# Kernel tuning notes

Measured on AMD Instinct MI355X. Metric: run time of the kernel, lower is better.

The kernel has to match this reference:

```python
import jax, jax.numpy as jnp
import numpy as np

B, L, D, H, NL = 4, 2048, 128, 4, 2
DH = D // H
FF = 2 * D
EPS_LN = 1e-5


def _p(key, shape, scale=0.05):
    return (jax.random.normal(key, shape, dtype=jnp.float32) * scale)


def setup_inputs() -> dict:
    key = jax.random.key(0)
    ks = jax.random.split(key, 40)
    inp = {
        "local_global": jax.random.normal(ks[0], (B, D), dtype=jnp.float32),
        "task_features": jax.random.normal(ks[1], (B, L, 15), dtype=jnp.float32),
        "privacy_features": jax.random.normal(ks[2], (B, L, 6), dtype=jnp.float32),
        "dag_features": jax.random.normal(ks[3], (B, L, 4), dtype=jnp.float32),
        # float mask in [0,1); values > 0.5 are MASKED (set to -inf) per torch code
        "attn_mask": jax.random.uniform(ks[4], (B, L, L), dtype=jnp.float32),
        # input projections (stored [in, out]; torch Linear does x @ W.T + b)
        "task_W": _p(ks[5], (15, D)), "task_b": jnp.zeros((D,), jnp.float32),
        "priv_W": _p(ks[6], (6, D)), "priv_b": jnp.zeros((D,), jnp.float32),
        "dag_W": _p(ks[7], (4, D)), "dag_b": jnp.zeros((D,), jnp.float32),
        "pre_g": jnp.ones((D,), jnp.float32), "pre_b": jnp.zeros((D,), jnp.float32),
        "post_g": jnp.ones((D,), jnp.float32), "post_b": jnp.zeros((D,), jnp.float32),
        "out_W": _p(ks[8], (D, D)), "out_b": jnp.zeros((D,), jnp.float32),
        # per-layer params stacked on leading NL axis
        "qW": _p(ks[9], (NL, D, D)), "qb": jnp.zeros((NL, D), jnp.float32),
        "kW": _p(ks[10], (NL, D, D)), "kb": jnp.zeros((NL, D), jnp.float32),
        "vW": _p(ks[11], (NL, D, D)), "vb": jnp.zeros((NL, D), jnp.float32),
        "oW": _p(ks[12], (NL, D, D)), "ob": jnp.zeros((NL, D), jnp.float32),
        "n1g": jnp.ones((NL, D), jnp.float32), "n1b": jnp.zeros((NL, D), jnp.float32),
        "n2g": jnp.ones((NL, D), jnp.float32), "n2b": jnp.zeros((NL, D), jnp.float32),
        "f1W": _p(ks[13], (NL, D, FF)), "f1b": jnp.zeros((NL, FF), jnp.float32),
        "f2W": _p(ks[14], (NL, FF, D)), "f2b": jnp.zeros((NL, D), jnp.float32),
    }
    return inp


def _layernorm(x, g, b):
    mu = x.mean(-1, keepdims=True)
    var = ((x - mu) ** 2).mean(-1, keepdims=True)
    return (x - mu) * jax.lax.rsqrt(var + EPS_LN) * g + b


def _attention(x, add_mask, Wq, bq, Wk, bk, Wv, bv, Wo, bo):
    # x: [B,L,D]; add_mask: [B,L,L] additive (0 or -inf)
    def heads(y):
        return y.reshape(B, L, H, DH).transpose(0, 2, 1, 3)  # [B,H,L,DH]
    q = heads(x @ Wq + bq)
    k = heads(x @ Wk + bk)
    v = heads(x @ Wv + bv)
    scale = 1.0 / np.sqrt(DH).astype(np.float32)
    scores = jnp.einsum('bhqd,bhkd->bhqk', q, k) * scale + add_mask[:, None]
    # fully-masked-row diagonal fixup (torch: set diag score to 0 where row max is -inf)
    row_max = scores.max(-1)                       # [B,H,L]
    fully_masked = jnp.isinf(row_max) & (row_max < 0)
    eye = jnp.eye(L, dtype=bool)
    scores = jnp.where(fully_masked[..., None] & eye, 0.0, scores)
    w = jax.nn.softmax(scores, axis=-1)
    # NaN fallback: if any NaN, replace with 1/L and renormalize (applied globally, as torch does)
    has_nan = jnp.isnan(w).any()
    fixed = jnp.nan_to_num(w, nan=1.0 / L)
    fixed = fixed / (fixed.sum(-1, keepdims=True) + 1e-8)
    w = jnp.where(has_nan, fixed, w)
    out = jnp.einsum('bhqk,bhkd->bhqd', w, v)      # [B,H,L,DH]
    out = out.transpose(0, 2, 1, 3).reshape(B, L, D)
    return out @ Wo + bo


def reference(local_global, task_features, privacy_features, dag_features, attn_mask,
              task_W, task_b, priv_W, priv_b, dag_W, dag_b,
              pre_g, pre_b, post_g, post_b, out_W, out_b,
              qW, qb, kW, kb, vW, vb, oW, ob,
              n1g, n1b, n2g, n2b, f1W, f1b, f2W, f2b):
    # normalize mask: >0.5 means masked; fix all-False rows by masking their diagonal (torch quirk)
    mb = attn_mask > 0.5                            # [B,L,L] bool, True = mask out
    need_fix = ~mb.any(-1)                          # [B,L]
    eye = jnp.eye(L, dtype=bool)
    mb = mb | (need_fix[..., None] & eye)
    add_mask = jnp.where(mb, -jnp.inf, 0.0).astype(jnp.float32)

    ctx = (task_features @ task_W + task_b) + (privacy_features @ priv_W + priv_b) \
          + (dag_features @ dag_W + dag_b)
    x = _layernorm(ctx, pre_g, pre_b)
    for i in range(NL):  # eval mode: dropout = identity
        sa = _attention(_layernorm(x, n1g[i], n1b[i]), add_mask,
                        qW[i], qb[i], kW[i], kb[i], vW[i], vb[i], oW[i], ob[i])
        x = x + sa
        h = _layernorm(x, n2g[i], n2b[i])
        ff = jax.nn.gelu(h @ f1W[i] + f1b[i], approximate=False) @ f2W[i] + f2b[i]
        x = x + ff
    enc = _layernorm(x, post_g, post_b)
    global_ctx = enc.mean(axis=1)                   # [B,D]
    fused = global_ctx + 0.1 * local_global
    aligned = fused @ out_W + out_b
    return aligned
```

## Files before the change

kernel.cpp:

```cpp
#include <hip/hip_runtime.h>
#include <hip/hip_bf16.h>

#define DEV __device__ __forceinline__

typedef float f32x4 __attribute__((ext_vector_type(4)));
typedef float f32x16 __attribute__((ext_vector_type(16)));
typedef short s16x8 __attribute__((ext_vector_type(8)));
typedef unsigned short u16x4 __attribute__((ext_vector_type(4)));
typedef __bf16 bf16x8 __attribute__((ext_vector_type(8)));

DEV bf16x8 as_bf16(s16x8 v) { return __builtin_bit_cast(bf16x8, v); }

DEV unsigned short f2bf(float f) {
    union { __hip_bfloat16 h; unsigned short u; } c;
    c.h = __float2bfloat16(f);
    return c.u;
}

DEV unsigned f2bf2(float lo, float hi) {
    unsigned ulo = __builtin_bit_cast(unsigned, lo);
    unsigned uhi = __builtin_bit_cast(unsigned, hi);
    ulo = (ulo + 0x7fffu + ((ulo >> 16) & 1u)) >> 16;
    uhi = (uhi + 0x7fffu + ((uhi >> 16) & 1u)) & 0xffff0000u;
    return ulo | uhi;
// ... 167 lines not shown
        for (int ns = 0; ns < 4; ++ns) {
            const int n = n0 + ns * 16 + c16;
            const float bv = bias[n];
            u16x4 pk;
#pragma unroll
            for (int r = 0; r < 4; ++r) pk[r] = f2bf(acc[ns][r] + bv);
            *(u16x4*)&vtbuf[(size_t)(n - 256) * 8192 + row0] = pk;
        }
        return;
    }
#pragma unroll
    for (int ns = 0; ns < 4; ++ns) {
        const int n = n0 + ns * 16 + c16;
        const float bv = bias[n];
#pragma unroll
        for (int r = 0; r < 4; ++r)
            qk[(size_t)(m0 + 4 * g + r) * 256 + n] = f2bf(acc[ns][r] + bv);
    }
}

__global__ __launch_bounds__(512) void gace_flash7_k(
    const unsigned short* __restrict__ QK,
    const unsigned short* __restrict__ Vt,
    const unsigned long long* __restrict__ bits,
    float* __restrict__ Op, float* __restrict__ ml)
{
    __shared__ __align__(16) unsigned short Ks[2 * 2 * 2560];
    __shared__ __align__(16) char VtB[2 * 2 * 4096];

    const int tid = threadIdx.x;
    const int wid = tid >> 6, l = tid & 63;
    const int c32 = l & 31, hi = l >> 5;
    const int bid = (blockIdx.x & 7) * 64 + (blockIdx.x >> 3);
    const int split = bid & 3, qc = (bid >> 2) & 7, h = (bid >> 5) & 3, b = bid >> 7;
    const size_t base = (size_t)b * 2048;
    const int qb0 = qc * 256 + wid * 32;
    const int q = qb0 + c32;

    const unsigned short* qrow = &QK[(base + q) * 256 + h * 32];
    const s16x8 qf0 = *(const s16x8*)&qrow[8 * hi];
    const s16x8 qf1 = *(const s16x8*)&qrow[16 + 8 * hi];
    const int rot3c = rot3(c32 & 7);

    f32x16 oacc;
#pragma unroll
    for (int i = 0; i < 16; ++i) oacc[i] = 0.f;
    float l_ = 0.f;

    const int st = tid & 255;
    const int sr = st >> 2;
    const int se = (tid & 3) << 3;
    const int lowr = sr & 31, t12 = lowr & 12;
    const int prow = (sr & 32) | (((t12 == 4) | (t12 == 8)) ? (lowr ^ 12) : lowr);
    const int rv = st >> 3;
    const int sv = tid & 7;
    const int vds = rv * 128 + 16 * (sv ^ rot3(rv & 7));

    const int kv0 = split * 512;
    const unsigned long long* bq = &bits[(base + q) * 32 + split * 8];
    const unsigned short* kgb = &QK[base * 256 + 128 + h * 32 + se];
    const unsigned short* vgb = &Vt[(size_t)(h * 32 + rv) * 8192 + base + kv0 + sv * 8];

    s16x8 kregA, kregB, vregA, vregB;
    auto LOAD = [&](int it2) {
        if (tid < 256) {
            const int kv = kv0 + it2 * 128;
            kregA = *(const s16x8*)&kgb[(size_t)(kv + sr) * 256];
            kregB = *(const s16x8*)&kgb[(size_t)(kv + 64 + sr) * 256];
        } else {
            vregA = *(const s16x8*)&vgb[it2 * 128];
            vregB = *(const s16x8*)&vgb[it2 * 128 + 64];
        }
    };
    auto STAGE = [&](int pb) {
        if (tid < 256) {
            *(s16x8*)&Ks[(pb * 2 + 0) * 2560 + prow * 40 + se] = kregA;
            *(s16x8*)&Ks[(pb * 2 + 1) * 2560 + prow * 40 + se] = kregB;
        } else {
            *(s16x8*)&VtB[(pb * 2 + 0) * 4096 + vds] = vregA;
            *(s16x8*)&VtB[(pb * 2 + 1) * 4096 + vds] = vregB;
        }
    };
    auto COMPUTE = [&](int pb, int sub, unsigned long long wb) {
        const unsigned short* KsS = &Ks[(pb * 2 + sub) * 2560];
        const char* VtS = &VtB[(pb * 2 + sub) * 4096];
        const unsigned long long wbs = wb >> (8 * hi);
        const unsigned wlo = (unsigned)wbs, whiw = (unsigned)(wbs >> 32);
        __builtin_amdgcn_s_setprio(1);
#pragma unroll
        for (int H = 0; H < 2; ++H) {
            const unsigned short* kr = &KsS[(32 * H + c32) * 40 + 8 * hi];
            f32x16 zv;
#pragma unroll
            for (int i = 0; i < 16; ++i) zv[i] = 0.f;
            f32x16 sac = __builtin_amdgcn_mfma_f32_32x32x16_bf16(
                as_bf16(*(const s16x8*)&kr[0]), as_bf16(qf0), zv, 0, 0, 0);
            sac = __builtin_amdgcn_mfma_f32_32x32x16_bf16(
                as_bf16(*(const s16x8*)&kr[16]), as_bf16(qf1), sac, 0, 0, 0);
            const unsigned word = (H == 0) ? wlo : whiw;
#pragma unroll
            for (int ch = 0; ch < 2; ++ch) {
                const int c = 2 * H + ch;
                const int bb = ch * 16;
                float p[8];
#pragma unroll
                for (int e = 0; e < 8; ++e) {
                    const float pe = exp2f(sac[ch * 8 + e]);
                    p[e] = ((word >> (bb + e)) & 1u) ? 0.f : pe;
                }
                l_ += ((p[0] + p[1]) + (p[2] + p[3])) + ((p[4] + p[5]) + (p[6] + p[7]));
                union { s16x8 v; unsigned d[4]; } pa;
#pragma unroll
                for (int j = 0; j < 4; ++j)
                    asm("v_cvt_pk_bf16_f32 %0, %1, %2"
                        : "=v"(pa.d[j]) : "v"(p[2 * j]), "v"(p[2 * j + 1]));
                const s16x8 vf = *(const s16x8*)&VtS[c32 * 128 + 16 * ((2 * c + hi) ^ rot3c)];
                oacc = __builtin_amdgcn_mfma_f32_32x32x16_bf16(
                    as_bf16(pa.v), as_bf16(vf), oacc, 0, 0, 0);
            }
        }
        __builtin_amdgcn_s_setprio(0);
    };

    unsigned long long wbv[8];
#pragma unroll
    for (int w = 0; w < 8; ++w) wbv[w] = bq[w];
    LOAD(0);
    STAGE(0);
    LOAD(1);
    __syncthreads();

#pragma unroll
    for (int it = 0; it < 4; ++it) {
        const int p = it & 1;
        COMPUTE(p, 0, wbv[2 * it]);
        if (it < 3) {
            STAGE(p ^ 1);
            if (it < 2) LOAD(it + 2);
        }
        COMPUTE(p, 1, wbv[2 * it + 1]);
        if (it < 3) __syncthreads();
    }

    l_ += __shfl_xor(l_, 32, 64);
    float* orow = &Op[((size_t)split * 8192 + base + qb0) * 128 + h * 32 + c32];
#pragma unroll
    for (int r = 0; r < 16; ++r) {
        const int qoff = (r & 3) + 8 * (r >> 2) + 4 * hi;
        orow[(size_t)qoff * 128] = oacc[r];
    }
    if (l < 32) ml[((size_t)split * 8192 + base + q) * 4 + h] = l_;
}

template<int LAST>
__global__ __launch_bounds__(128) void gace_post_k(
    const float* __restrict__ Op, const float* __restrict__ ml,
    const unsigned short* __restrict__ oWt, const float* __restrict__ obv,
    float* __restrict__ x,
    const float* __restrict__ n2g, const float* __restrict__ n2b,
    const unsigned short* __restrict__ f1Wt, const float* __restrict__ f1b,
    const unsigned short* __restrict__ f2Wt, const float* __restrict__ f2b,
    const float* __restrict__ post_g, const float* __restrict__ post_b,
    float* __restrict__ partial)
{
    __shared__ __align__(16) float xbuf[2][16][132];
    __shared__ __align__(16) unsigned short g1buf[2][16][264];
    __shared__ float red[2][128];
    const int tid = threadIdx.x, wid = tid >> 6, l = tid & 63;
    const int g = (l >> 4) & 3, c16 = l & 15;
    const int m0 = blockIdx.x * 32 + wid * 16;
    const int arow = m0 + c16;

    s16x8 af[4];
#pragma unroll
    for (int kc = 0; kc < 4; ++kc) {
        float o[8];
#pragma unroll
        for (int e = 0; e < 8; ++e) o[e] = 0.f;
        float Ls = 0.f;
#pragma unroll
        for (int sp = 0; sp < 4; ++sp) {
            const size_t ro = (size_t)sp * 8192 + arow;
            const f32x4 a0 = *(const f32x4*)&Op[ro * 128 + kc * 32 + 8 * g];
            const f32x4 a1 = *(const f32x4*)&Op[ro * 128 + kc * 32 + 8 * g + 4];
#pragma unroll
            for (int e = 0; e < 4; ++e) { o[e] += a0[e]; o[4 + e] += a1[e]; }
            Ls += ml[ro * 4 + kc];
        }
        const float inv = 1.f / Ls;
        union { s16x8 v8; unsigned d[4]; } pk;
#pragma unroll
        for (int j = 0; j < 4; ++j) pk.d[j] = f2bf2(o[2 * j] * inv, o[2 * j + 1] * inv);
        af[kc] = pk.v8;
    }
    f32x4 acc8[8];
#pragma unroll
    for (int i = 0; i < 8; ++i) acc8[i] = f32x4{0.f, 0.f, 0.f, 0.f};
#pragma unroll
    for (int ns = 0; ns < 8; ++ns) {
        const unsigned short* wrow = oWt + (size_t)(16 * ns + c16) * 128;
#pragma unroll
        for (int kc = 0; kc < 4; ++kc)
            acc8[ns] = __builtin_amdgcn_mfma_f32_16x16x32_bf16(
                as_bf16(af[kc]), as_bf16(*(const s16x8*)&wrow[kc * 32 + 8 * g]),
                acc8[ns], 0, 0, 0);
    }
#pragma unroll
    for (int ns = 0; ns < 8; ++ns) {
        const int n = 16 * ns + c16;
        const float bv = obv[n];
#pragma unroll
        for (int r = 0; r < 4; ++r) {
            const int lr = 4 * g + r;
            xbuf[wid][lr][n] = acc8[ns][r] + bv + x[(size_t)(m0 + lr) * 128 + n];
        }
    }
    float v2[4][8];
#pragma unroll
    for (int kc = 0; kc < 4; ++kc) {
        const f32x4 a0 = *(const f32x4*)&xbuf[wid][c16][kc * 32 + 8 * g];
        const f32x4 a1 = *(const f32x4*)&xbuf[wid][c16][kc * 32 + 8 * g + 4];
#pragma unroll
        for (int e = 0; e < 4; ++e) { v2[kc][e] = a0[e]; v2[kc][4 + e] = a1[e]; }
    }
    float s = 0.f;
#pragma unroll
    for (int kc = 0; kc < 4; ++kc)
#pragma unroll
        for (int e = 0; e < 8; ++e) s += v2[kc][e];
    s += __shfl_xor(s, 16, 64); s += __shfl_xor(s, 32, 64);
    const float mean = s * (1.f / 128.f);
    float s2 = 0.f;
#pragma unroll
    for (int kc = 0; kc < 4; ++kc)
#pragma unroll
        for (int e = 0; e < 8; ++e) { const float d = v2[kc][e] - mean; s2 += d * d; }
    s2 += __shfl_xor(s2, 16, 64); s2 += __shfl_xor(s2, 32, 64);
    const float rs = rsqrtf(s2 * (1.f / 128.f) + 1e-5f);
    s16x8 af1[4];
#pragma unroll
    for (int kc = 0; kc < 4; ++kc) {
        union { s16x8 v8; unsigned d[4]; } pk;
#pragma unroll
        for (int j = 0; j < 4; ++j) {
            const int col = kc * 32 + 8 * g + 2 * j;
            const float x0 = (v2[kc][2 * j] - mean) * rs * n2g[col] + n2b[col];
            const float x1 = (v2[kc][2 * j + 1] - mean) * rs * n2g[col + 1] + n2b[col + 1];
            pk.d[j] = f2bf2(x0, x1);
        }
        af1[kc] = pk.v8;
    }
    f32x4 acc16[16];
#pragma unroll
    for (int i = 0; i < 16; ++i) acc16[i] = f32x4{0.f, 0.f, 0.f, 0.f};
#pragma unroll
    for (int ns = 0; ns < 16; ++ns) {
        const unsigned short* wrow = f1Wt + (size_t)(16 * ns + c16) * 128;
#pragma unroll
        for (int kc = 0; kc < 4; ++kc)
            acc16[ns] = __builtin_amdgcn_mfma_f32_16x16x32_bf16(
                as_bf16(af1[kc]), as_bf16(*(const s16x8*)&wrow[kc * 32 + 8 * g]),
                acc16[ns], 0, 0, 0);
    }
#pragma unroll
    for (int ns = 0; ns < 16; ++ns) {
        const int n = 16 * ns + c16;
        const float bv = f1b[n];
#pragma unroll
        for (int r = 0; r < 4; ++r) {
            float vv = acc16[ns][r] + bv;
            vv = vv * 0.5f * (1.0f + erff(vv * 0.70710678118654752f));
            g1buf[wid][4 * g + r][n] = f2bf(vv);
        }
    }
    s16x8 af2[8];
#pragma unroll
    for (int kc = 0; kc < 8; ++kc)
        af2[kc] = *(const s16x8*)&g1buf[wid][c16][kc * 32 + 8 * g];
    f32x4 acc8b[8];
#pragma unroll
    for (int i = 0; i < 8; ++i) acc8b[i] = f32x4{0.f, 0.f, 0.f, 0.f};
#pragma unroll
    for (int ns = 0; ns < 8; ++ns) {
        const unsigned short* wrow = f2Wt + (size_t)(16 * ns + c16) * 256;
#pragma unroll
        for (int kc = 0; kc < 8; ++kc)
            acc8b[ns] = __builtin_amdgcn_mfma_f32_16x16x32_bf16(
                as_bf16(af2[kc]), as_bf16(*(const s16x8*)&wrow[kc * 32 + 8 * g]),
                acc8b[ns], 0, 0, 0);
    }
    float fx[8][4];
#pragma unroll
    for (int ns = 0; ns < 8; ++ns) {
        const int n = 16 * ns + c16;
        const float bv = f2b[n];
#pragma unroll
        for (int r = 0; r < 4; ++r)
            fx[ns][r] = acc8b[ns][r] + bv + xbuf[wid][4 * g + r][n];
    }
    if (!LAST) {
#pragma unroll
        for (int ns = 0; ns < 8; ++ns) {
            const int n = 16 * ns + c16;
#pragma unroll
            for (int r = 0; r < 4; ++r)
                x[(size_t)(m0 + 4 * g + r) * 128 + n] = fx[ns][r];
        }
        return;
    }
    float colsum[8];
#pragma unroll
    for (int ns = 0; ns < 8; ++ns) colsum[ns] = 0.f;
#pragma unroll
    for (int r = 0; r < 4; ++r) {
        float sr_ = 0.f;
#pragma unroll
        for (int ns = 0; ns < 8; ++ns) sr_ += fx[ns][r];
        sr_ += __shfl_xor(sr_, 1, 64); sr_ += __shfl_xor(sr_, 2, 64);
        sr_ += __shfl_xor(sr_, 4, 64); sr_ += __shfl_xor(sr_, 8, 64);
        const float mr = sr_ * (1.f / 128.f);
        float vr = 0.f;
#pragma unroll
        for (int ns = 0; ns < 8; ++ns) { const float d = fx[ns][r] - mr; vr += d * d; }
        vr += __shfl_xor(vr, 1, 64); vr += __shfl_xor(vr, 2, 64);
        vr += __shfl_xor(vr, 4, 64); vr += __shfl_xor(vr, 8, 64);
        const float rsr = rsqrtf(vr * (1.f / 128.f) + 1e-5f);
#pragma unroll
        for (int ns = 0; ns < 8; ++ns) {
            const int n = 16 * ns + c16;
            colsum[ns] += (fx[ns][r] - mr) * rsr * post_g[n] + post_b[n];
        }
    }
#pragma unroll
    for (int ns = 0; ns < 8; ++ns) {
        colsum[ns] += __shfl_xor(colsum[ns], 16, 64);
        colsum[ns] += __shfl_xor(colsum[ns], 32, 64);
    }
    if (l < 16) {
#pragma unroll
        for (int ns = 0; ns < 8; ++ns) red[wid][16 * ns + c16] = colsum[ns];
    }
    __syncthreads();
    if (tid < 128)
        partial[(size_t)blockIdx.x * 128 + tid] = red[0][tid] + red[1][tid];
}

__global__ __launch_bounds__(128) void gace_tailB_k(
    const float* __restrict__ partial, const float* __restrict__ lg,
    const float* __restrict__ oW, const float* __restrict__ obv,
    float* __restrict__ out)
{
    const int tid = threadIdx.x, b2 = blockIdx.x;
    __shared__ float fused[128];
    float s = 0.f;
#pragma unroll 8
    for (int c = 0; c < 64; ++c) s += partial[(size_t)(b2 * 64 + c) * 128 + tid];
    fused[tid] = s * (1.f / 2048.f) + 0.1f * lg[b2 * 128 + tid];
    __syncthreads();
    float r = obv[tid];
#pragma unroll 8
    for (int d2 = 0; d2 < 128; ++d2) r += fused[d2] * oW[d2 * 128 + tid];
    out[b2 * 128 + tid] = r;
}

extern "C" void kernel_launch(void* const* d_in, const int* in_sizes, int n_in,
                              void* d_out, int out_size, void* d_ws, size_t ws_size,
                              hipStream_t stream)
{
    (void)in_sizes; (void)n_in; (void)out_size; (void)ws_size;
    const float* local_global = (const float*)d_in[0];
    const float* task   = (const float*)d_in[1];
    const float* priv   = (const float*)d_in[2];
    const float* dag    = (const float*)d_in[3];
    const float* amask  = (const float*)d_in[4];
    const float* task_W = (const float*)d_in[5];
    const float* task_b = (const float*)d_in[6];
    const float* priv_W = (const float*)d_in[7];
    const float* priv_b = (const float*)d_in[8];
    const float* dag_W  = (const float*)d_in[9];
    const float* dag_b  = (const float*)d_in[10];
    const float* pre_g  = (const float*)d_in[11];
    const float* pre_b  = (const float*)d_in[12];
    const float* post_g = (const float*)d_in[13];
    const float* post_b = (const float*)d_in[14];
    const float* out_W  = (const float*)d_in[15];
    const float* out_b  = (const float*)d_in[16];
    const float* qW = (const float*)d_in[17];
    const float* qb = (const float*)d_in[18];
    const float* kW = (const float*)d_in[19];
    const float* kb = (const float*)d_in[20];
    const float* vW = (const float*)d_in[21];
    const float* vb = (const float*)d_in[22];
    const float* oW = (const float*)d_in[23];
    const float* ob = (const float*)d_in[24];
    const float* n1g = (const float*)d_in[25];
    const float* n1b = (const float*)d_in[26];
    const float* n2g = (const float*)d_in[27];
    const float* n2b = (const float*)d_in[28];
    const float* f1W = (const float*)d_in[29];
    const float* f1b = (const float*)d_in[30];
    const float* f2W = (const float*)d_in[31];
    const float* f2b = (const float*)d_in[32];

    char* ws = (char*)d_ws;
    size_t off = 0;
    auto carve = [&](size_t sz) {
        void* p = ws + off;
        off += (sz + 255) & ~(size_t)255;
        return p;
    };
    unsigned long long* bits = (unsigned long long*)carve(8192ull * 32 * 8);
    float*          x    = (float*)carve(8192ull * 128 * 4);
    unsigned short* qk   = (unsigned short*)carve(8192ull * 256 * 2);
    unsigned short* vt   = (unsigned short*)carve(128ull * 8192 * 2);
    float*          part = (float*)carve(256ull * 128 * 4);
    float*          Op   = (float*)carve(4ull * 8192 * 128 * 4);
    float*          mlb  = (float*)carve(4ull * 8192 * 4 * 4);
    unsigned short* wbf  = (unsigned short*)carve(2ull * 131072 * 2);
    float*          bcat = (float*)carve(2ull * 384 * 4);

    gace_setup_k<<<5888, 256, 0, stream>>>(
        amask, bits,
        task, priv, dag, task_W, task_b, priv_W, priv_b, dag_W, dag_b,
        pre_g, pre_b, x,
        qW, kW, vW, oW, f1W, f2W, qb, kb, vb, wbf, bcat);
    for (int i = 0; i < 2; ++i) {
        const unsigned short* wl = wbf + (size_t)i * 131072;
        gace_qkv_k<<<dim3(128, 6), 256, 0, stream>>>(
            x, n1g + i * 128, n1b + i * 128, wl, bcat + i * 384, qk, vt);
        gace_flash7_k<<<512, 512, 0, stream>>>(qk, vt, bits, Op, mlb);
        if (i == 0)
            gace_post_k<0><<<256, 128, 0, stream>>>(
                Op, mlb, wl + 49152, ob, x, n2g, n2b,
                wl + 65536, f1b, wl + 98304, f2b, post_g, post_b, part);
        else
            gace_post_k<1><<<256, 128, 0, stream>>>(
                Op, mlb, wl + 49152, ob + 128, x, n2g + 128, n2b + 128,
                wl + 65536, f1b + 256, wl + 98304, f2b + 128, post_g, post_b, part);
    }
    gace_tailB_k<<<4, 128, 0, stream>>>(part, local_global, out_W, out_b, (float*)d_out);
}
```

Measured before the change: 175.5 us.

## Fuse layer-0 post-attention MLP with layer-1 LayerNorm and QKV projection

Adds a kernel that, after the layer-0 attention merge, out-projection and FFN, also computes the layer-1 LayerNorm and QKV projection for its rows and writes q/k and transposed v directly. This removes one kernel launch and the re-read of x by a separate QKV kernel between layers. The fused kernel runs on only 256 blocks of 128 threads, so the QKV work gets less parallelism than the dedicated 128x6 grid had. Register pressure also rises in the longer kernel.

New measurement: 169.7 us. 3.3% less time.

```diff
diff --git a/kernel.cpp b/kernel.cpp
--- a/kernel.cpp
+++ b/kernel.cpp
@@ -343,7 +343,229 @@
     if (l < 32) ml[((size_t)split * 8192 + base + q) * 4 + h] = l_;
 }
 
-template<int LAST>
+__global__ __launch_bounds__(128) void gace_postqkv_k(
+    const float* __restrict__ Op, const float* __restrict__ ml,
+    const unsigned short* __restrict__ oWt, const float* __restrict__ obv,
+    float* __restrict__ x,
+    const float* __restrict__ n2g, const float* __restrict__ n2b,
+    const unsigned short* __restrict__ f1Wt, const float* __restrict__ f1b,
+    const unsigned short* __restrict__ f2Wt, const float* __restrict__ f2b,
+    const float* __restrict__ n1g2, const float* __restrict__ n1b2,
+    const unsigned short* __restrict__ w2,
+    const float* __restrict__ bcat2,
+    unsigned short* __restrict__ qk, unsigned short* __restrict__ vtbuf)
+{
+    __shared__ __align__(16) float xbuf[2][16][132];
+    __shared__ __align__(16) unsigned short g1buf[2][16][264];
+    const int tid = threadIdx.x, wid = tid >> 6, l = tid & 63;
+    const int g = (l >> 4) & 3, c16 = l & 15;
+    const int m0 = blockIdx.x * 32 + wid * 16;
+    const int arow = m0 + c16;
+
+    s16x8 af[4];
+#pragma unroll
+    for (int kc = 0; kc < 4; ++kc) {
+        float o[8];
+#pragma unroll
+        for (int e = 0; e < 8; ++e) o[e] = 0.f;
+        float Ls = 0.f;
+#pragma unroll
+        for (int sp = 0; sp < 4; ++sp) {
+            const size_t ro = (size_t)sp * 8192 + arow;
+            const f32x4 a0 = *(const f32x4*)&Op[ro * 128 + kc * 32 + 8 * g];
+            const f32x4 a1 = *(const f32x4*)&Op[ro * 128 + kc * 32 + 8 * g + 4];
+#pragma unroll
+            for (int e = 0; e < 4; ++e) { o[e] += a0[e]; o[4 + e] += a1[e]; }
+            Ls += ml[ro * 4 + kc];
+        }
+        const float inv = 1.f / Ls;
+        union { s16x8 v8; unsigned d[4]; } pk;
+#pragma unroll
+        for (int j = 0; j < 4; ++j) pk.d[j] = f2bf2(o[2 * j] * inv, o[2 * j + 1] * inv);
+        af[kc] = pk.v8;
+    }
+    f32x4 acc8[8];
+#pragma unroll
+    for (int i = 0; i < 8; ++i) acc8[i] = f32x4{0.f, 0.f, 0.f, 0.f};
+#pragma unroll
+    for (int ns = 0; ns < 8; ++ns) {
+        const unsigned short* wrow = oWt + (size_t)(16 * ns + c16) * 128;
+#pragma unroll
+        for (int kc = 0; kc < 4; ++kc)
+            acc8[ns] = __builtin_amdgcn_mfma_f32_16x16x32_bf16(
+                as_bf16(af[kc]), as_bf16(*(const s16x8*)&wrow[kc * 32 + 8 * g]),
+                acc8[ns], 0, 0, 0);
+    }
+#pragma unroll
+    for (int ns = 0; ns < 8; ++ns) {
+        const int n = 16 * ns + c16;
+        const float bv = obv[n];
+#pragma unroll
+        for (int r = 0; r < 4; ++r) {
+            const int lr = 4 * g + r;
+            xbuf[wid][lr][n] = acc8[ns][r] + bv + x[(size_t)(m0 + lr) * 128 + n];
+        }
+    }
+    float v2[4][8];
+#pragma unroll
+    for (int kc = 0; kc < 4; ++kc) {
+        const f32x4 a0 = *(const f32x4*)&xbuf[wid][c16][kc * 32 + 8 * g];
+        const f32x4 a1 = *(const f32x4*)&xbuf[wid][c16][kc * 32 + 8 * g + 4];
+#pragma unroll
+        for (int e = 0; e < 4; ++e) { v2[kc][e] = a0[e]; v2[kc][4 + e] = a1[e]; }
+    }
+    float s = 0.f;
+#pragma unroll
+    for (int kc = 0; kc < 4; ++kc)
+#pragma unroll
+        for (int e = 0; e < 8; ++e) s += v2[kc][e];
+    s += __shfl_xor(s, 16, 64); s += __shfl_xor(s, 32, 64);
+    const float mean = s * (1.f / 128.f);
+    float s2 = 0.f;
+#pragma unroll
+    for (int kc = 0; kc < 4; ++kc)
+#pragma unroll
+        for (int e = 0; e < 8; ++e) { const float d = v2[kc][e] - mean; s2 += d * d; }
+    s2 += __shfl_xor(s2, 16, 64); s2 += __shfl_xor(s2, 32, 64);
+    const float rs = rsqrtf(s2 * (1.f / 128.f) + 1e-5f);
+    s16x8 af1[4];
+#pragma unroll
+    for (int kc = 0; kc < 4; ++kc) {
+        union { s16x8 v8; unsigned d[4]; } pk;
+#pragma unroll
+        for (int j = 0; j < 4; ++j) {
+            const int col = kc * 32 + 8 * g + 2 * j;
+            const float x0 = (v2[kc][2 * j] - mean) * rs * n2g[col] + n2b[col];
+            const float x1 = (v2[kc][2 * j + 1] - mean) * rs * n2g[col + 1] + n2b[col + 1];
+            pk.d[j] = f2bf2(x0, x1);
+        }
+        af1[kc] = pk.v8;
+    }
+    f32x4 acc16[16];
+#pragma unroll
+    for (int i = 0; i < 16; ++i) acc16[i] = f32x4{0.f, 0.f, 0.f, 0.f};
+#pragma unroll
+    for (int ns = 0; ns < 16; ++ns) {
+        const unsigned short* wrow = f1Wt + (size_t)(16 * ns + c16) * 128;
+#pragma unroll
+        for (int kc = 0; kc < 4; ++kc)
+            acc16[ns] = __builtin_amdgcn_mfma_f32_16x16x32_bf16(
+                as_bf16(af1[kc]), as_bf16(*(const s16x8*)&wrow[kc * 32 + 8 * g]),
+                acc16[ns], 0, 0, 0);
+    }
+#pragma unroll
+    for (int ns = 0; ns < 16; ++ns) {
+        const int n = 16 * ns + c16;
+        const float bv = f1b[n];
+#pragma unroll
+        for (int r = 0; r < 4; ++r) {
+            float vv = acc16[ns][r] + bv;
+            vv = vv * 0.5f * (1.0f + erff(vv * 0.70710678118654752f));
+            g1buf[wid][4 * g + r][n] = f2bf(vv);
+        }
+    }
+    s16x8 af2[8];
+#pragma unroll
+    for (int kc = 0; kc < 8; ++kc)
+        af2[kc] = *(const s16x8*)&g1buf[wid][c16][kc * 32 + 8 * g];
+    f32x4 acc8b[8];
+#pragma unroll
+    for (int i = 0; i < 8; ++i) acc8b[i] = f32x4{0.f, 0.f, 0.f, 0.f};
+#pragma unroll
+    for (int ns = 0; ns < 8; ++ns) {
+        const unsigned short* wrow = f2Wt + (size_t)(16 * ns + c16) * 256;
+#pragma unroll
+        for (int kc = 0; kc < 8; ++kc)
+            acc8b[ns] = __builtin_amdgcn_mfma_f32_16x16x32_bf16(
+                as_bf16(af2[kc]), as_bf16(*(const s16x8*)&wrow[kc * 32 + 8 * g]),
+                acc8b[ns], 0, 0, 0);
+    }
+#pragma unroll
+    for (int ns = 0; ns < 8; ++ns) {
+        const int n = 16 * ns + c16;
+        const float bv = f2b[n];
+#pragma unroll
+        for (int r = 0; r < 4; ++r) {
+            const int lr = 4 * g + r;
+            const float fxv = acc8b[ns][r] + bv + xbuf[wid][lr][n];
+            x[(size_t)(m0 + lr) * 128 + n] = fxv;
+            xbuf[wid][lr][n] = fxv;
+        }
+    }
+    float v1[4][8];
+#pragma unroll
+    for (int kc = 0; kc < 4; ++kc) {
+        const f32x4 a0 = *(const f32x4*)&xbuf[wid][c16][kc * 32 + 8 * g];
+        const f32x4 a1 = *(const f32x4*)&xbuf[wid][c16][kc * 32 + 8 * g + 4];
+#pragma unroll
+        for (int e = 0; e < 4; ++e) { v1[kc][e] = a0[e]; v1[kc][4 + e] = a1[e]; }
+    }
+    float s1 = 0.f;
+#pragma unroll
+    for (int kc = 0; kc < 4; ++kc)
+#pragma unroll
+        for (int e = 0; e < 8; ++e) s1 += v1[kc][e];
+    s1 += __shfl_xor(s1, 16, 64); s1 += __shfl_xor(s1, 32, 64);
+    const float mean1 = s1 * (1.f / 128.f);
+    float sq1 = 0.f;
+#pragma unroll
+    for (int kc = 0; kc < 4; ++kc)
+#pragma unroll
+        for (int e = 0; e < 8; ++e) { const float d = v1[kc][e] - mean1; sq1 += d * d; }
+    sq1 += __shfl_xor(sq1, 16, 64); sq1 += __shfl_xor(sq1, 32, 64);
+    const float rs1 = rsqrtf(sq1 * (1.f / 128.f) + 1e-5f);
+    s16x8 afq[4];
+#pragma unroll
+    for (int kc = 0; kc < 4; ++kc) {
+        union { s16x8 v8; unsigned d[4]; } pk;
+#pragma unroll
+        for (int j = 0; j < 4; ++j) {
+            const int col = kc * 32 + 8 * g + 2 * j;
+            const float x0 = (v1[kc][2 * j] - mean1) * rs1 * n1g2[col] + n1b2[col];
+            const float x1 = (v1[kc][2 * j + 1] - mean1) * rs1 * n1g2[col + 1] + n1b2[col + 1];
+            pk.d[j] = f2bf2(x0, x1);
+        }
+        afq[kc] = pk.v8;
+    }
+#pragma unroll
+    for (int nt = 0; nt < 6; ++nt) {
+        const int n0 = nt * 64;
+        f32x4 acc[4];
+#pragma unroll
+        for (int z = 0; z < 4; ++z) acc[z] = f32x4{0.f, 0.f, 0.f, 0.f};
+#pragma unroll
+        for (int ns = 0; ns < 4; ++ns) {
+            const unsigned short* wrow = w2 + (size_t)(n0 + 16 * ns + c16) * 128;
+#pragma unroll
+            for (int kc = 0; kc < 4; ++kc)
+                acc[ns] = __builtin_amdgcn_mfma_f32_16x16x32_bf16(
+                    as_bf16(afq[kc]), as_bf16(*(const s16x8*)&wrow[kc * 32 + 8 * g]),
+                    acc[ns], 0, 0, 0);
+        }
+        if (n0 >= 256) {
+            const int row0 = m0 + 4 * g;
+#pragma unroll
+            for (int ns = 0; ns < 4; ++ns) {
+                const int n = n0 + ns * 16 + c16;
+                const float bv = bcat2[n];
+                u16x4 pk;
+#pragma unroll
+                for (int r = 0; r < 4; ++r) pk[r] = f2bf(acc[ns][r] + bv);
+                *(u16x4*)&vtbuf[(size_t)(n - 256) * 8192 + row0] = pk;
+            }
+        } else {
+#pragma unroll
+            for (int ns = 0; ns < 4; ++ns) {
+                const int n = n0 + ns * 16 + c16;
+                const float bv = bcat2[n];
+#pragma unroll
+                for (int r = 0; r < 4; ++r)
+                    qk[(size_t)(m0 + 4 * g + r) * 256 + n] = f2bf(acc[ns][r] + bv);
+            }
+        }
+    }
+}
+
 __global__ __launch_bounds__(128) void gace_post_k(
     const float* __restrict__ Op, const float* __restrict__ ml,
     const unsigned short* __restrict__ oWt, const float* __restrict__ obv,
@@ -488,16 +710,6 @@
 #pragma unroll
         for (int r = 0; r < 4; ++r)
             fx[ns][r] = acc8b[ns][r] + bv + xbuf[wid][4 * g + r][n];
-    }
-    if (!LAST) {
-#pragma unroll
-        for (int ns = 0; ns < 8; ++ns) {
-            const int n = 16 * ns + c16;
-#pragma unroll
-            for (int r = 0; r < 4; ++r)
-                x[(size_t)(m0 + 4 * g + r) * 128 + n] = fx[ns][r];
-        }
-        return;
     }
     float colsum[8];
 #pragma unroll
@@ -615,19 +827,17 @@
         task, priv, dag, task_W, task_b, priv_W, priv_b, dag_W, dag_b,
         pre_g, pre_b, x,
         qW, kW, vW, oW, f1W, f2W, qb, kb, vb, wbf, bcat);
-    for (int i = 0; i < 2; ++i) {
-        const unsigned short* wl = wbf + (size_t)i * 131072;
-        gace_qkv_k<<<dim3(128, 6), 256, 0, stream>>>(
-            x, n1g + i * 128, n1b + i * 128, wl, bcat + i * 384, qk, vt);
-        gace_flash7_k<<<512, 512, 0, stream>>>(qk, vt, bits, Op, mlb);
-        if (i == 0)
-            gace_post_k<0><<<256, 128, 0, stream>>>(
-                Op, mlb, wl + 49152, ob, x, n2g, n2b,
-                wl + 65536, f1b, wl + 98304, f2b, post_g, post_b, part);
-        else
-            gace_post_k<1><<<256, 128, 0, stream>>>(
-                Op, mlb, wl + 49152, ob + 128, x, n2g + 128, n2b + 128,
-                wl + 65536, f1b + 256, wl + 98304, f2b + 128, post_g, post_b, part);
-    }
+    gace_qkv_k<<<dim3(128, 6), 256, 0, stream>>>(
+        x, n1g, n1b, wbf, bcat, qk, vt);
+    gace_flash7_k<<<512, 512, 0, stream>>>(qk, vt, bits, Op, mlb);
+    gace_postqkv_k<<<256, 128, 0, stream>>>(
+        Op, mlb, wbf + 49152, ob, x, n2g, n2b,
+        wbf + 65536, f1b, wbf + 98304, f2b,
+        n1g + 128, n1b + 128, wbf + 131072, bcat + 384, qk, vt);
+    gace_flash7_k<<<512, 512, 0, stream>>>(qk, vt, bits, Op, mlb);
+    gace_post_k<<<256, 128, 0, stream>>>(
+        Op, mlb, wbf + 131072 + 49152, ob + 128, x, n2g + 128, n2b + 128,
+        wbf + 131072 + 65536, f1b + 256, wbf + 131072 + 98304, f2b + 128,
+        post_g, post_b, part);
     gace_tailB_k<<<4, 128, 0, stream>>>(part, local_global, out_W, out_b, (float*)d_out);
 }
```

## Fuse layer-2 QKV projection into layer-1 post kernel and split N across waves

Applied to the files above, without the earlier changes.

The post-attention kernel now processes 16 rows per block with 4 waves that split the output columns, instead of each wave owning 16 rows with all columns. For layer 1 it also applies the next layer's LayerNorm and QKV projection, writing qk/vt directly and removing one separate QKV launch. The final LN and column-sum path is rewritten for the new layout, and the tail reduction now reads 128 partials per batch. This doubles the grid and adds block-level syncs in exchange for more parallelism and one fewer launch and x re-read.

Result: faster. 160.7 us (-8.5%).

```diff
diff --git a/kernel.cpp b/kernel.cpp
--- a/kernel.cpp
+++ b/kernel.cpp
@@ -343,23 +343,26 @@
     if (l < 32) ml[((size_t)split * 8192 + base + q) * 4 + h] = l_;
 }
 
-template<int LAST>
-__global__ __launch_bounds__(128) void gace_post_k(
+template<int QKV, int LAST>
+__global__ __launch_bounds__(256) void gace_post2_k(
     const float* __restrict__ Op, const float* __restrict__ ml,
     const unsigned short* __restrict__ oWt, const float* __restrict__ obv,
     float* __restrict__ x,
     const float* __restrict__ n2g, const float* __restrict__ n2b,
     const unsigned short* __restrict__ f1Wt, const float* __restrict__ f1b,
     const unsigned short* __restrict__ f2Wt, const float* __restrict__ f2b,
+    const float* __restrict__ n1g2, const float* __restrict__ n1b2,
+    const unsigned short* __restrict__ w2, const float* __restrict__ bcat2,
+    unsigned short* __restrict__ qk, unsigned short* __restrict__ vtbuf,
     const float* __restrict__ post_g, const float* __restrict__ post_b,
     float* __restrict__ partial)
 {
-    __shared__ __align__(16) float xbuf[2][16][132];
-    __shared__ __align__(16) unsigned short g1buf[2][16][264];
-    __shared__ float red[2][128];
+    __shared__ __align__(16) float xbuf[16][132];
+    __shared__ __align__(16) unsigned short g1buf[16][264];
+    __shared__ float stats[16][2];
     const int tid = threadIdx.x, wid = tid >> 6, l = tid & 63;
     const int g = (l >> 4) & 3, c16 = l & 15;
-    const int m0 = blockIdx.x * 32 + wid * 16;
+    const int m0 = blockIdx.x * 16;
     const int arow = m0 + c16;
 
     s16x8 af[4];
@@ -384,156 +387,238 @@
         for (int j = 0; j < 4; ++j) pk.d[j] = f2bf2(o[2 * j] * inv, o[2 * j + 1] * inv);
         af[kc] = pk.v8;
     }
-    f32x4 acc8[8];
-#pragma unroll
-    for (int i = 0; i < 8; ++i) acc8[i] = f32x4{0.f, 0.f, 0.f, 0.f};
-#pragma unroll
-    for (int ns = 0; ns < 8; ++ns) {
-        const unsigned short* wrow = oWt + (size_t)(16 * ns + c16) * 128;
+    {
+        f32x4 acc2[2];
+#pragma unroll
+        for (int z = 0; z < 2; ++z) acc2[z] = f32x4{0.f, 0.f, 0.f, 0.f};
+#pragma unroll
+        for (int nsl = 0; nsl < 2; ++nsl) {
+            const int ns = wid * 2 + nsl;
+            const unsigned short* wrow = oWt + (size_t)(16 * ns + c16) * 128;
+#pragma unroll
+            for (int kc = 0; kc < 4; ++kc)
+                acc2[nsl] = __builtin_amdgcn_mfma_f32_16x16x32_bf16(
+                    as_bf16(af[kc]), as_bf16(*(const s16x8*)&wrow[kc * 32 + 8 * g]),
+                    acc2[nsl], 0, 0, 0);
+        }
+#pragma unroll
+        for (int nsl = 0; nsl < 2; ++nsl) {
+            const int n = 16 * (wid * 2 + nsl) + c16;
+            const float bv = obv[n];
+#pragma unroll
+            for (int r = 0; r < 4; ++r) {
+                const int lr = 4 * g + r;
+                xbuf[lr][n] = acc2[nsl][r] + bv + x[(size_t)(m0 + lr) * 128 + n];
+            }
+        }
+    }
+    __syncthreads();
+    s16x8 af1[4];
+    {
+        float v2[4][8];
+#pragma unroll
+        for (int kc = 0; kc < 4; ++kc) {
+            const f32x4 a0 = *(const f32x4*)&xbuf[c16][kc * 32 + 8 * g];
+            const f32x4 a1 = *(const f32x4*)&xbuf[c16][kc * 32 + 8 * g + 4];
+#pragma unroll
+            for (int e = 0; e < 4; ++e) { v2[kc][e] = a0[e]; v2[kc][4 + e] = a1[e]; }
+        }
+        float s = 0.f;
 #pragma unroll
         for (int kc = 0; kc < 4; ++kc)
-            acc8[ns] = __builtin_amdgcn_mfma_f32_16x16x32_bf16(
-                as_bf16(af[kc]), as_bf16(*(const s16x8*)&wrow[kc * 32 + 8 * g]),
-                acc8[ns], 0, 0, 0);
-    }
-#pragma unroll
-    for (int ns = 0; ns < 8; ++ns) {
-        const int n = 16 * ns + c16;
-        const float bv = obv[n];
+#pragma unroll
+            for (int e = 0; e < 8; ++e) s += v2[kc][e];
+        s += __shfl_xor(s, 16, 64); s += __shfl_xor(s, 32, 64);
+        const float mean = s * (1.f / 128.f);
+        float s2 = 0.f;
+#pragma unroll
+        for (int kc = 0; kc < 4; ++kc)
+#pragma unroll
+            for (int e = 0; e < 8; ++e) { const float d = v2[kc][e] - mean; s2 += d * d; }
+        s2 += __shfl_xor(s2, 16, 64); s2 += __shfl_xor(s2, 32, 64);
+        const float rs = rsqrtf(s2 * (1.f / 128.f) + 1e-5f);
+#pragma unroll
+        for (int kc = 0; kc < 4; ++kc) {
+            union { s16x8 v8; unsigned d[4]; } pk;
+#pragma unroll
+            for (int j = 0; j < 4; ++j) {
+                const int col = kc * 32 + 8 * g + 2 * j;
+                const float x0 = (v2[kc][2 * j] - mean) * rs * n2g[col] + n2b[col];
+                const float x1 = (v2[kc][2 * j + 1] - mean) * rs * n2g[col + 1] + n2b[col + 1];
+                pk.d[j] = f2bf2(x0, x1);
+            }
+            af1[kc] = pk.v8;
+        }
+    }
+    {
+        f32x4 accf[4];
+#pragma unroll
+        for (int z = 0; z < 4; ++z) accf[z] = f32x4{0.f, 0.f, 0.f, 0.f};
+#pragma unroll
+        for (int nsl = 0; nsl < 4; ++nsl) {
+            const int ns = wid * 4 + nsl;
+            const unsigned short* wrow = f1Wt + (size_t)(16 * ns + c16) * 128;
+#pragma unroll
+            for (int kc = 0; kc < 4; ++kc)
+                accf[nsl] = __builtin_amdgcn_mfma_f32_16x16x32_bf16(
+                    as_bf16(af1[kc]), as_bf16(*(const s16x8*)&wrow[kc * 32 + 8 * g]),
+                    accf[nsl], 0, 0, 0);
+        }
+#pragma unroll
+        for (int nsl = 0; nsl < 4; ++nsl) {
+            const int n = 16 * (wid * 4 + nsl) + c16;
+            const float bv = f1b[n];
+#pragma unroll
+            for (int r = 0; r < 4; ++r) {
+                float vv = accf[nsl][r] + bv;
+                vv = vv * 0.5f * (1.0f + erff(vv * 0.70710678118654752f));
+                g1buf[4 * g + r][n] = f2bf(vv);
+            }
+        }
+    }
+    __syncthreads();
+    float fx[2][4];
+    {
+        s16x8 af2[8];
+#pragma unroll
+        for (int kc = 0; kc < 8; ++kc)
+            af2[kc] = *(const s16x8*)&g1buf[c16][kc * 32 + 8 * g];
+        f32x4 acc2[2];
+#pragma unroll
+        for (int z = 0; z < 2; ++z) acc2[z] = f32x4{0.f, 0.f, 0.f, 0.f};
+#pragma unroll
+        for (int nsl = 0; nsl < 2; ++nsl) {
+            const int ns = wid * 2 + nsl;
+            const unsigned short* wrow = f2Wt + (size_t)(16 * ns + c16) * 256;
+#pragma unroll
+            for (int kc = 0; kc < 8; ++kc)
+                acc2[nsl] = __builtin_amdgcn_mfma_f32_16x16x32_bf16(
+                    as_bf16(af2[kc]), as_bf16(*(const s16x8*)&wrow[kc * 32 + 8 * g]),
+                    acc2[nsl], 0, 0, 0);
+        }
+#pragma unroll
+        for (int nsl = 0; nsl < 2; ++nsl) {
+            const int n = 16 * (wid * 2 + nsl) + c16;
+            const float bv = f2b[n];
+#pragma unroll
+            for (int r = 0; r < 4; ++r)
+                fx[nsl][r] = acc2[nsl][r] + bv + xbuf[4 * g + r][n];
+        }
+    }
+    if (!QKV && !LAST) {
+#pragma unroll
+        for (int nsl = 0; nsl < 2; ++nsl) {
+            const int n = 16 * (wid * 2 + nsl) + c16;
+#pragma unroll
+            for (int r = 0; r < 4; ++r)
+                x[(size_t)(m0 + 4 * g + r) * 128 + n] = fx[nsl][r];
+        }
+        return;
+    }
+#pragma unroll
+    for (int nsl = 0; nsl < 2; ++nsl) {
+        const int n = 16 * (wid * 2 + nsl) + c16;
 #pragma unroll
         for (int r = 0; r < 4; ++r) {
             const int lr = 4 * g + r;
-            xbuf[wid][lr][n] = acc8[ns][r] + bv + x[(size_t)(m0 + lr) * 128 + n];
-        }
-    }
-    float v2[4][8];
-#pragma unroll
-    for (int kc = 0; kc < 4; ++kc) {
-        const f32x4 a0 = *(const f32x4*)&xbuf[wid][c16][kc * 32 + 8 * g];
-        const f32x4 a1 = *(const f32x4*)&xbuf[wid][c16][kc * 32 + 8 * g + 4];
-#pragma unroll
-        for (int e = 0; e < 4; ++e) { v2[kc][e] = a0[e]; v2[kc][4 + e] = a1[e]; }
-    }
-    float s = 0.f;
-#pragma unroll
-    for (int kc = 0; kc < 4; ++kc)
-#pragma unroll
-        for (int e = 0; e < 8; ++e) s += v2[kc][e];
-    s += __shfl_xor(s, 16, 64); s += __shfl_xor(s, 32, 64);
-    const float mean = s * (1.f / 128.f);
-    float s2 = 0.f;
-#pragma unroll
-    for (int kc = 0; kc < 4; ++kc)
-#pragma unroll
-        for (int e = 0; e < 8; ++e) { const float d = v2[kc][e] - mean; s2 += d * d; }
-    s2 += __shfl_xor(s2, 16, 64); s2 += __shfl_xor(s2, 32, 64);
-    const float rs = rsqrtf(s2 * (1.f / 128.f) + 1e-5f);
-    s16x8 af1[4];
-#pragma unroll
-    for (int kc = 0; kc < 4; ++kc) {
-        union { s16x8 v8; unsigned d[4]; } pk;
-#pragma unroll
-        for (int j = 0; j < 4; ++j) {
-            const int col = kc * 32 + 8 * g + 2 * j;
-            const float x0 = (v2[kc][2 * j] - mean) * rs * n2g[col] + n2b[col];
-            const float x1 = (v2[kc][2 * j + 1] - mean) * rs * n2g[col + 1] + n2b[col + 1];
-            pk.d[j] = f2bf2(x0, x1);
-        }
-        af1[kc] = pk.v8;
-    }
-    f32x4 acc16[16];
-#pragma unroll
-    for (int i = 0; i < 16; ++i) acc16[i] = f32x4{0.f, 0.f, 0.f, 0.f};
-#pragma unroll
-    for (int ns = 0; ns < 16; ++ns) {
-        const unsigned short* wrow = f1Wt + (size_t)(16 * ns + c16) * 128;
-#pragma unroll
-        for (int kc = 0; kc < 4; ++kc)
-            acc16[ns] = __builtin_amdgcn_mfma_f32_16x16x32_bf16(
-                as_bf16(af1[kc]), as_bf16(*(const s16x8*)&wrow[kc * 32 + 8 * g]),
-                acc16[ns], 0, 0, 0);
-    }
-#pragma unroll
-    for (int ns = 0; ns < 16; ++ns) {
-        const int n = 16 * ns + c16;
-        const float bv = f1b[n];
-#pragma unroll
-        for (int r = 0; r < 4; ++r) {
-            float vv = acc16[ns][r] + bv;
-            vv = vv * 0.5f * (1.0f + erff(vv * 0.70710678118654752f));
-            g1buf[wid][4 * g + r][n] = f2bf(vv);
-        }
-    }
-    s16x8 af2[8];
-#pragma unroll
-    for (int kc = 0; kc < 8; ++kc)
-        af2[kc] = *(const s16x8*)&g1buf[wid][c16][kc * 32 + 8 * g];
-    f32x4 acc8b[8];
-#pragma unroll
-    for (int i = 0; i < 8; ++i) acc8b[i] = f32x4{0.f, 0.f, 0.f, 0.f};
-#pragma unroll
-    for (int ns = 0; ns < 8; ++ns) {
-        const unsigned short* wrow = f2Wt + (size_t)(16 * ns + c16) * 256;
-#pragma unroll
-        for (int kc = 0; kc < 8; ++kc)
-            acc8b[ns] = __builtin_amdgcn_mfma_f32_16x16x32_bf16(
-                as_bf16(af2[kc]), as_bf16(*(const s16x8*)&wrow[kc * 32 + 8 * g]),
-                acc8b[ns], 0, 0, 0);
-    }
-    float fx[8][4];
-#pragma unroll
-    for (int ns = 0; ns < 8; ++ns) {
-        const int n = 16 * ns + c16;
-        const float bv = f2b[n];
-#pragma unroll
-        for (int r = 0; r < 4; ++r)
-            fx[ns][r] = acc8b[ns][r] + bv + xbuf[wid][4 * g + r][n];
-    }
-    if (!LAST) {
-#pragma unroll
-        for (int ns = 0; ns < 8; ++ns) {
+            if (QKV) x[(size_t)(m0 + lr) * 128 + n] = fx[nsl][r];
+            xbuf[lr][n] = fx[nsl][r];
+        }
+    }
+    __syncthreads();
+    if (QKV) {
+        s16x8 afq[4];
+        {
+            float v1[4][8];
+#pragma unroll
+            for (int kc = 0; kc < 4; ++kc) {
+                const f32x4 a0 = *(const f32x4*)&xbuf[c16][kc * 32 + 8 * g];
+                const f32x4 a1 = *(const f32x4*)&xbuf[c16][kc * 32 + 8 * g + 4];
+#pragma unroll
+                for (int e = 0; e < 4; ++e) { v1[kc][e] = a0[e]; v1[kc][4 + e] = a1[e]; }
+            }
+            float s1 = 0.f;
+#pragma unroll
+            for (int kc = 0; kc < 4; ++kc)
+#pragma unroll
+                for (int e = 0; e < 8; ++e) s1 += v1[kc][e];
+            s1 += __shfl_xor(s1, 16, 64); s1 += __shfl_xor(s1, 32, 64);
+            const float mean1 = s1 * (1.f / 128.f);
+            float sq1 = 0.f;
+#pragma unroll
+            for (int kc = 0; kc < 4; ++kc)
+#pragma unroll
+                for (int e = 0; e < 8; ++e) { const float d = v1[kc][e] - mean1; sq1 += d * d; }
+            sq1 += __shfl_xor(sq1, 16, 64); sq1 += __shfl_xor(sq1, 32, 64);
+            const float rs1 = rsqrtf(sq1 * (1.f / 128.f) + 1e-5f);
+#pragma unroll
+            for (int kc = 0; kc < 4; ++kc) {
+                union { s16x8 v8; unsigned d[4]; } pk;
+#pragma unroll
+                for (int j = 0; j < 4; ++j) {
+                    const int col = kc * 32 + 8 * g + 2 * j;
+                    const float x0 = (v1[kc][2 * j] - mean1) * rs1 * n1g2[col] + n1b2[col];
+                    const float x1 = (v1[kc][2 * j + 1] - mean1) * rs1 * n1g2[col + 1] + n1b2[col + 1];
+                    pk.d[j] = f2bf2(x0, x1);
+                }
+                afq[kc] = pk.v8;
+            }
+        }
+#pragma unroll
+        for (int j = 0; j < 6; ++j) {
+            const int ns = wid * 6 + j;
+            const unsigned short* wrow = w2 + (size_t)(ns * 16 + c16) * 128;
+            f32x4 acc = f32x4{0.f, 0.f, 0.f, 0.f};
+#pragma unroll
+            for (int kc = 0; kc < 4; ++kc)
+                acc = __builtin_amdgcn_mfma_f32_16x16x32_bf16(
+                    as_bf16(afq[kc]), as_bf16(*(const s16x8*)&wrow[kc * 32 + 8 * g]),
+                    acc, 0, 0, 0);
+            const int n = ns * 16 + c16;
+            const float bv = bcat2[n];
+            if (ns >= 16) {
+                const int row0 = m0 + 4 * g;
+                u16x4 pk;
+#pragma unroll
+                for (int r = 0; r < 4; ++r) pk[r] = f2bf(acc[r] + bv);
+                *(u16x4*)&vtbuf[(size_t)(n - 256) * 8192 + row0] = pk;
+            } else {
+#pragma unroll
+                for (int r = 0; r < 4; ++r)
+                    qk[(size_t)(m0 + 4 * g + r) * 256 + n] = f2bf(acc[r] + bv);
+            }
+        }
+        return;
+    }
+    {
+#pragma unroll
+        for (int rr = 0; rr < 4; ++rr) {
+            const int row = wid * 4 + rr;
+            const float v0 = xbuf[row][l], v1 = xbuf[row][l + 64];
+            const float s = wave_sum64(v0 + v1);
+            const float mean = s * (1.f / 128.f);
+            const float d0 = v0 - mean, d1 = v1 - mean;
+            const float s2 = wave_sum64(d0 * d0 + d1 * d1);
+            const float rstd = rsqrtf(s2 * (1.f / 128.f) + 1e-5f);
+            if (l == 0) { stats[row][0] = mean; stats[row][1] = rstd; }
+        }
+        __syncthreads();
+#pragma unroll
+        for (int nsl = 0; nsl < 2; ++nsl) {
+            const int ns = wid * 2 + nsl;
             const int n = 16 * ns + c16;
-#pragma unroll
-            for (int r = 0; r < 4; ++r)
-                x[(size_t)(m0 + 4 * g + r) * 128 + n] = fx[ns][r];
-        }
-        return;
-    }
-    float colsum[8];
-#pragma unroll
-    for (int ns = 0; ns < 8; ++ns) colsum[ns] = 0.f;
-#pragma unroll
-    for (int r = 0; r < 4; ++r) {
-        float sr_ = 0.f;
-#pragma unroll
-        for (int ns = 0; ns < 8; ++ns) sr_ += fx[ns][r];
-        sr_ += __shfl_xor(sr_, 1, 64); sr_ += __shfl_xor(sr_, 2, 64);
-        sr_ += __shfl_xor(sr_, 4, 64); sr_ += __shfl_xor(sr_, 8, 64);
-        const float mr = sr_ * (1.f / 128.f);
-        float vr = 0.f;
-#pragma unroll
-        for (int ns = 0; ns < 8; ++ns) { const float d = fx[ns][r] - mr; vr += d * d; }
-        vr += __shfl_xor(vr, 1, 64); vr += __shfl_xor(vr, 2, 64);
-        vr += __shfl_xor(vr, 4, 64); vr += __shfl_xor(vr, 8, 64);
-        const float rsr = rsqrtf(vr * (1.f / 128.f) + 1e-5f);
-#pragma unroll
-        for (int ns = 0; ns < 8; ++ns) {
-            const int n = 16 * ns + c16;
-            colsum[ns] += (fx[ns][r] - mr) * rsr * post_g[n] + post_b[n];
-        }
-    }
-#pragma unroll
-    for (int ns = 0; ns < 8; ++ns) {
-        colsum[ns] += __shfl_xor(colsum[ns], 16, 64);
-        colsum[ns] += __shfl_xor(colsum[ns], 32, 64);
-    }
-    if (l < 16) {
-#pragma unroll
-        for (int ns = 0; ns < 8; ++ns) red[wid][16 * ns + c16] = colsum[ns];
-    }
-    __syncthreads();
-    if (tid < 128)
-        partial[(size_t)blockIdx.x * 128 + tid] = red[0][tid] + red[1][tid];
+            const float pg = post_g[n], pb_ = post_b[n];
+            float cs = 0.f;
+#pragma unroll
+            for (int r = 0; r < 4; ++r) {
+                const int row = 4 * g + r;
+                cs += (xbuf[row][n] - stats[row][0]) * stats[row][1] * pg + pb_;
+            }
+            cs += __shfl_xor(cs, 16, 64);
+            cs += __shfl_xor(cs, 32, 64);
+            if (l < 16) partial[(size_t)blockIdx.x * 128 + n] = cs;
+        }
+    }
 }
 
 __global__ __launch_bounds__(128) void gace_tailB_k(
@@ -545,7 +630,7 @@
     __shared__ float fused[128];
     float s = 0.f;
 #pragma unroll 8
-    for (int c = 0; c < 64; ++c) s += partial[(size_t)(b2 * 64 + c) * 128 + tid];
+    for (int c = 0; c < 128; ++c) s += partial[(size_t)(b2 * 128 + c) * 128 + tid];
     fused[tid] = s * (1.f / 2048.f) + 0.1f * lg[b2 * 128 + tid];
     __syncthreads();
     float r = obv[tid];
@@ -604,7 +689,7 @@
     float*          x    = (float*)carve(8192ull * 128 * 4);
     unsigned short* qk   = (unsigned short*)carve(8192ull * 256 * 2);
     unsigned short* vt   = (unsigned short*)carve(128ull * 8192 * 2);
-    float*          part = (float*)carve(256ull * 128 * 4);
+    float*          part = (float*)carve(512ull * 128 * 4);
     float*          Op   = (float*)carve(4ull * 8192 * 128 * 4);
     float*          mlb  = (float*)carve(4ull * 8192 * 4 * 4);
     unsigned short* wbf  = (unsigned short*)carve(2ull * 131072 * 2);
@@ -615,19 +700,19 @@
         task, priv, dag, task_W, task_b, priv_W, priv_b, dag_W, dag_b,
         pre_g, pre_b, x,
         qW, kW, vW, oW, f1W, f2W, qb, kb, vb, wbf, bcat);
-    for (int i = 0; i < 2; ++i) {
-        const unsigned short* wl = wbf + (size_t)i * 131072;
-        gace_qkv_k<<<dim3(128, 6), 256, 0, stream>>>(
-            x, n1g + i * 128, n1b + i * 128, wl, bcat + i * 384, qk, vt);
-        gace_flash7_k<<<512, 512, 0, stream>>>(qk, vt, bits, Op, mlb);
-        if (i == 0)
-            gace_post_k<0><<<256, 128, 0, stream>>>(
-                Op, mlb, wl + 49152, ob, x, n2g, n2b,
-                wl + 65536, f1b, wl + 98304, f2b, post_g, post_b, part);
-        else
-            gace_post_k<1><<<256, 128, 0, stream>>>(
-                Op, mlb, wl + 49152, ob + 128, x, n2g + 128, n2b + 128,
-                wl + 65536, f1b + 256, wl + 98304, f2b + 128, post_g, post_b, part);
-    }
+    gace_qkv_k<<<dim3(128, 6), 256, 0, stream>>>(
+        x, n1g, n1b, wbf, bcat, qk, vt);
+    gace_flash7_k<<<512, 512, 0, stream>>>(qk, vt, bits, Op, mlb);
+    gace_post2_k<1, 0><<<512, 256, 0, stream>>>(
+        Op, mlb, wbf + 49152, ob, x, n2g, n2b,
+        wbf + 65536, f1b, wbf + 98304, f2b,
+        n1g + 128, n1b + 128, wbf + 131072, bcat + 384, qk, vt,
+        nullptr, nullptr, nullptr);
+    gace_flash7_k<<<512, 512, 0, stream>>>(qk, vt, bits, Op, mlb);
+    gace_post2_k<0, 1><<<512, 256, 0, stream>>>(
+        Op, mlb, wbf + 131072 + 49152, ob + 128, x, n2g + 128, n2b + 128,
+        wbf + 131072 + 65536, f1b + 256, wbf + 131072 + 98304, f2b + 128,
+        nullptr, nullptr, nullptr, nullptr, nullptr, nullptr,
+        post_g, post_b, part);
     gace_tailB_k<<<4, 128, 0, stream>>>(part, local_global, out_W, out_b, (float*)d_out);
 }
```
